# Kernel tuning notes

Measured on AMD Instinct MI355X. Metric: run time of the kernel, lower is better.

## Reference

```python
import jax, jax.numpy as jnp
import numpy as np

MARGIN = 0.3
EPS = 1e-12

def setup_inputs() -> dict:
    key = jax.random.key(0)
    k1, k2 = jax.random.split(key)
    B, D, NUM_IDS = 1024, 2048, 256
    features = jax.random.normal(k1, (B, D), dtype=jnp.float32)
    labels = jax.random.randint(k2, (B,), 0, NUM_IDS, dtype=jnp.int64)
    return {"features": features, "labels": labels}

def _pairwise_euclidean(features):
    # dist^2 = |x_i|^2 + |x_j|^2 - 2 x_i . x_j, clamped then sqrt (as in torch ref)
    sq = jnp.sum(features * features, axis=1)  # [B]
    d2 = sq[:, None] + sq[None, :] - 2.0 * (features @ features.T)
    return jnp.sqrt(jnp.maximum(d2, EPS))

def reference(features, labels):
    B = features.shape[0]
    dist = _pairwise_euclidean(features)  # [B, B]
    eq = labels[None, :] == labels[:, None]  # [B, B]; eq[i] == labels_equal row i
    eye = jnp.eye(B, dtype=bool)
    pos_mask = eq & ~eye
    neg_mask = ~eq
    neg_inf = jnp.float32(-jnp.inf)
    pos_inf = jnp.float32(jnp.inf)
    hardest_pos = jnp.max(jnp.where(pos_mask, dist, neg_inf), axis=1)  # [B]
    hardest_neg = jnp.min(jnp.where(neg_mask, dist, pos_inf), axis=1)  # [B]
    valid = jnp.any(pos_mask, axis=1) & jnp.any(neg_mask, axis=1)  # rows contributing a triplet
    per_row = jax.nn.relu(hardest_pos - hardest_neg + MARGIN)
    per_row = jnp.where(valid, per_row, 0.0)
    n_valid = jnp.sum(valid)
    loss = jnp.sum(per_row) / jnp.maximum(n_valid, 1).astype(per_row.dtype)
    num_active = jnp.sum(valid & (per_row > 0))
    return loss, num_active
```

## Files before the change

### kernel.cpp

```cpp
#include <hip/hip_runtime.h>
#include <math.h>

#define B_SZ 1024
#define D_SZ 2048
#define MARGIN 0.3f

typedef _Float16 f16x8 __attribute__((ext_vector_type(8)));
typedef float f32x16 __attribute__((ext_vector_type(16)));

union FragU { uint4 u; f16x8 v; };
union H4 { _Float16 h[4]; uint2 u; };



__global__ __launch_bounds__(256) void prep_kernel(const float* __restrict__ F,
                                                   _Float16* __restrict__ Fh,
                                                   float* __restrict__ sqpart,
                                                   int* __restrict__ hp,
                                                   int* __restrict__ hn,
                                                   int* __restrict__ flags) {
    __shared__ _Float16 slab[64][136];
    __shared__ float part[64];

    const int b = blockIdx.x;
    const int i = b >> 4;
    const int kseg = b & 15;
    const int t = threadIdx.x;
    const int lane = t & 63;
    const int w = t >> 6;

    const int idx = b * 256 + t;
    if (idx < 1024) {
        hp[idx] = 0;
        hn[idx] = 0x7F800000;
        flags[idx] = 0;
    }

#pragma unroll
    for (int q = 0; q < 8; ++q) {
        const int rl = q * 8 + (t >> 5);
        const int c4 = (t & 31) * 4;
        const float4 v = *(const float4*)(F + (size_t)(i * 64 + rl) * D_SZ +
                                          kseg * 128 + c4);
        float s = v.x * v.x + v.y * v.y + v.z * v.z + v.w * v.w;
#pragma unroll
        for (int mask = 1; mask < 32; mask <<= 1) s += __shfl_xor(s, mask);
        if ((t & 31) == 0) part[rl] = s;
        H4 p;
        p.h[0] = (_Float16)v.x; p.h[1] = (_Float16)v.y;
        p.h[2] = (_Float16)v.z; p.h[3] = (_Float16)v.w;
        *(uint2*)&slab[rl][c4] = p.u;
    }
    __syncthreads();

    if (t < 64) sqpart[kseg * 1024 + i * 64 + t] = part[t];

#pragma unroll
    for (int q2 = 0; q2 < 4; ++q2) {
        const int u = w * 4 + q2;
        const int kb = u >> 1;
        const int rg = u & 1;
        const uint4 d = *(const uint4*)&slab[rg * 32 + (lane & 31)]
                                          [kb * 16 + (lane >> 5) * 8];
        const size_t g = (size_t)((i * 128 + kseg * 8 + kb) * 2 + rg);
        *(uint4*)((char*)Fh + g * 1024 + (size_t)lane * 16) = d;
    }
}


__global__ __launch_bounds__(256, 2) void dist_f16_kernel(
    const _Float16* __restrict__ Fh, const int* __restrict__ labels,
    const float* __restrict__ sqpart, int* __restrict__ hp,
    int* __restrict__ hn, int* __restrict__ flags) {
    __shared__ __align__(16) char cb[32768];
    __shared__ int labR[64], labC[32];
    __shared__ float sqR[64], sqC[32];

    const int t = threadIdx.x;
    const int lane = t & 63;
    const int w = t >> 6;

    const int xcd = blockIdx.x & 7;
    const int cidx = blockIdx.x >> 3;
    const int bi = (xcd >> 1) * 4 + (cidx >> 4);
    const int bj = (xcd & 1) * 16 + (cidx & 15);
    const int rowBase = bi * 64, colBase = bj * 32;

    if (t < 64) {
        const int row = rowBase + t;
        float s = 0.f;
#pragma unroll
        for (int p = 0; p < 16; ++p) s += sqpart[p * 1024 + row];
        sqR[t] = s;
        labR[t] = labels[row];
    } else if (t < 96) {
        const int e = t - 64;
        const int row = colBase + e;
        float s = 0.f;
#pragma unroll
        for (int p = 0; p < 16; ++p) s += sqpart[p * 1024 + row];
        sqC[e] = s;
        labC[e] = labels[row];
    }
    __syncthreads();

    const char* __restrict__ FhB = (const char*)Fh;
    const char* pA0 = FhB + (size_t)((bi * 128 + w * 32) * 2) * 1024 + (size_t)lane * 16;
    const char* pB0 = FhB + (size_t)(((bj >> 1) * 128 + w * 32) * 2 + (bj & 1)) * 1024 +
                      (size_t)lane * 16;

    f32x16 acc[2];
#pragma unroll
    for (int a = 0; a < 2; ++a)
#pragma unroll
        for (int e = 0; e < 16; ++e) acc[a][e] = 0.f;

    auto LOADREG = [&](int s, uint4* r) {
        const size_t off = (size_t)s * 2048;
        r[0] = *(const uint4*)(pA0 + off);
        r[1] = *(const uint4*)(pA0 + off + 1024);
        r[2] = *(const uint4*)(pB0 + off);
    };
    auto MFMA2 = [&](const uint4* r) {
        FragU a0, a1, v0;
        a0.u = r[0];
        a1.u = r[1];
        v0.u = r[2];
        acc[0] = __builtin_amdgcn_mfma_f32_32x32x16_f16(a0.v, v0.v, acc[0], 0, 0, 0);
        acc[1] = __builtin_amdgcn_mfma_f32_32x32x16_f16(a1.v, v0.v, acc[1], 0, 0, 0);
    };

    uint4 ra[3], rb[3];
    LOADREG(0, ra);
#pragma unroll
    for (int s = 0; s < 32; s += 2) {
        LOADREG(s + 1, rb);
        MFMA2(ra);
        if (s + 2 < 32) LOADREG(s + 2, ra);
        MFMA2(rb);
    }

    __syncthreads();

#pragma unroll
    for (int fr = 0; fr < 2; ++fr)
#pragma unroll
        for (int g = 0; g < 4; ++g) {
            float4 v;
            v.x = acc[fr][g * 4 + 0];
            v.y = acc[fr][g * 4 + 1];
            v.z = acc[fr][g * 4 + 2];
            v.w = acc[fr][g * 4 + 3];
            *(float4*)(cb + (size_t)(w * 8192) +
                       (size_t)((fr * 4 + g) * 64 + lane) * 16) = v;
        }
    __syncthreads();

    if (w < 2) {
        const int fr = w;
        float cS[16];
#pragma unroll
        for (int e = 0; e < 16; ++e) cS[e] = 0.f;
#pragma unroll
        for (int wp = 0; wp < 4; ++wp)
#pragma unroll
            for (int g = 0; g < 4; ++g) {
                float4 v = *(const float4*)(cb + (size_t)(wp * 8192) +
                                            (size_t)((fr * 4 + g) * 64 + lane) * 16);
                cS[g * 4 + 0] += v.x;
                cS[g * 4 + 1] += v.y;
                cS[g * 4 + 2] += v.z;
                cS[g * 4 + 3] += v.w;
            }

        const float BIG = 1e38f;
        const int h = lane >> 5;
        const int colL = lane & 31;
        const int j = colBase + colL;
        const int lj = labC[colL];
        const float sqj = sqC[colL];
#pragma unroll
        for (int k = 0; k < 16; ++k) {
            const int rowL = fr * 32 + (k & 3) + 8 * (k >> 2) + 4 * h;
            const int i = rowBase + rowL;
            const float d2 = sqR[rowL] + sqj - 2.f * cS[k];
            const float d = sqrtf(fmaxf(d2, 1e-12f));
            const bool eq = (labR[rowL] == lj);
            const bool isPos = eq && (i != j);
            float pv = isPos ? d : -BIG;
            float nv = eq ? BIG : d;
            int pf = (isPos ? 1 : 0) | (eq ? 0 : 2);
#pragma unroll
            for (int mask = 1; mask < 32; mask <<= 1) {
                pv = fmaxf(pv, __shfl_xor(pv, mask));
                nv = fminf(nv, __shfl_xor(nv, mask));
                pf |= __shfl_xor(pf, mask);
            }
            if (colL == 0) {
                if (pf & 1) atomicMax(&hp[i], __float_as_int(pv));
                if (pf & 2) atomicMin(&hn[i], __float_as_int(nv));
                if (pf) atomicOr(&flags[i], pf);
            }
        }
    }
}


__global__ __launch_bounds__(1024) void final_kernel(const int* __restrict__ hp,
                                                     const int* __restrict__ hn,
                                                     const int* __restrict__ flags,
                                                     float* __restrict__ out) {
    __shared__ float ssum[16];
    __shared__ int svalid[16], sact[16];
    const int t = threadIdx.x;
    const float hpv = __int_as_float(hp[t]);
    const float hnv = __int_as_float(hn[t]);
    const int f = flags[t];
    const bool valid = (f == 3);
    float pr = fmaxf(hpv - hnv + MARGIN, 0.f);
    if (!valid) pr = 0.f;
    int act = (valid && pr > 0.f) ? 1 : 0;
    int vld = valid ? 1 : 0;
    float s = pr;
    for (int off = 32; off; off >>= 1) {
        s += __shfl_down(s, off);
        act += __shfl_down(act, off);
        vld += __shfl_down(vld, off);
    }
    if ((t & 63) == 0) {
        ssum[t >> 6] = s;
        svalid[t >> 6] = vld;
        sact[t >> 6] = act;
    }
    __syncthreads();
    if (t == 0) {
        float tot = 0.f;
        int nv = 0, na = 0;
#pragma unroll
        for (int i = 0; i < 16; ++i) {
            tot += ssum[i];
            nv += svalid[i];
            na += sact[i];
        }
        out[0] = tot / (float)(nv > 1 ? nv : 1);
        out[1] = (float)na;
    }
}


#define BM 64
#define BN 64
#define BK 32

__global__ __launch_bounds__(256) void sq_kernel(const float* __restrict__ F,
                                                 float* __restrict__ sq) {
    int row = blockIdx.x;
    const float4* r4 = (const float4*)(F + (size_t)row * D_SZ);
    int t = threadIdx.x;
    float s = 0.f;
#pragma unroll
    for (int q = 0; q < 2; ++q) {
        float4 v = r4[t + q * 256];
        s += v.x * v.x + v.y * v.y + v.z * v.z + v.w * v.w;
    }
    for (int off = 32; off; off >>= 1) s += __shfl_down(s, off);
    __shared__ float wsum[4];
    if ((t & 63) == 0) wsum[t >> 6] = s;
    __syncthreads();
    if (t == 0) sq[row] = wsum[0] + wsum[1] + wsum[2] + wsum[3];
}

__global__ __launch_bounds__(256) void init_kernel(int* __restrict__ hp,
                                                   int* __restrict__ hn,
                                                   int* __restrict__ flags) {
    int i = blockIdx.x * 256 + threadIdx.x;
    hp[i] = 0;
    hn[i] = 0x7F800000;
    flags[i] = 0;
}

__global__ __launch_bounds__(256) void dist_f32_kernel(
    const float* __restrict__ F, const int* __restrict__ labels,
    const float* __restrict__ sq, int* __restrict__ hp, int* __restrict__ hn,
    int* __restrict__ flags) {
    __shared__ float As[BK][BM];
    __shared__ float Bs[BK][BN];
    __shared__ int labR[BM], labC[BN];
    __shared__ float sqR[BM], sqC[BN];

    const int rowBase = blockIdx.y * BM;
    const int colBase = blockIdx.x * BN;
    const int t = threadIdx.x;
    const int tx = t & 15;
    const int ty = t >> 4;

    if (t < 64) {
        labR[t] = labels[rowBase + t];
        sqR[t] = sq[rowBase + t];
    } else if (t < 128) {
        int u = t - 64;
        labC[u] = labels[colBase + u];
        sqC[u] = sq[colBase + u];
    }

    float acc[4][4] = {{0.f}};
    const int m = t & 63;
    const int q = t >> 6;
    const float* aRow = F + (size_t)(rowBase + m) * D_SZ + q * 8;
    const float* bRow = F + (size_t)(colBase + m) * D_SZ + q * 8;

    for (int k0 = 0; k0 < D_SZ; k0 += BK) {
        float4 a0 = *(const float4*)(aRow + k0);
        float4 a1 = *(const float4*)(aRow + k0 + 4);
        float4 b0 = *(const float4*)(bRow + k0);
        float4 b1 = *(const float4*)(bRow + k0 + 4);
        __syncthreads();
        int kb = q * 8;
        As[kb + 0][m] = a0.x; As[kb + 1][m] = a0.y;
        As[kb + 2][m] = a0.z; As[kb + 3][m] = a0.w;
        As[kb + 4][m] = a1.x; As[kb + 5][m] = a1.y;
        As[kb + 6][m] = a1.z; As[kb + 7][m] = a1.w;
        Bs[kb + 0][m] = b0.x; Bs[kb + 1][m] = b0.y;
        Bs[kb + 2][m] = b0.z; Bs[kb + 3][m] = b0.w;
        Bs[kb + 4][m] = b1.x; Bs[kb + 5][m] = b1.y;
        Bs[kb + 6][m] = b1.z; Bs[kb + 7][m] = b1.w;
        __syncthreads();
#pragma unroll
        for (int kk = 0; kk < BK; ++kk) {
            float4 a = *(const float4*)&As[kk][ty * 4];
            float4 b = *(const float4*)&Bs[kk][tx * 4];
            acc[0][0] += a.x * b.x; acc[0][1] += a.x * b.y;
            acc[0][2] += a.x * b.z; acc[0][3] += a.x * b.w;
            acc[1][0] += a.y * b.x; acc[1][1] += a.y * b.y;
            acc[1][2] += a.y * b.z; acc[1][3] += a.y * b.w;
            acc[2][0] += a.z * b.x; acc[2][1] += a.z * b.y;
            acc[2][2] += a.z * b.z; acc[2][3] += a.z * b.w;
            acc[3][0] += a.w * b.x; acc[3][1] += a.w * b.y;
            acc[3][2] += a.w * b.z; acc[3][3] += a.w * b.w;
        }
    }

    float mp[4], mn[4];
    int pf[4];
#pragma unroll
    for (int rr = 0; rr < 4; ++rr) {
        const int i = rowBase + ty * 4 + rr;
        const int li = labR[ty * 4 + rr];
        const float si = sqR[ty * 4 + rr];
        mp[rr] = -3.4e38f;
        mn[rr] = 3.4e38f;
        pf[rr] = 0;
#pragma unroll
        for (int c = 0; c < 4; ++c) {
            const int j = colBase + tx * 4 + c;
            const float d2 = si + sqC[tx * 4 + c] - 2.f * acc[rr][c];
            const float dist = sqrtf(fmaxf(d2, 1e-12f));
            const bool eq = (li == labC[tx * 4 + c]);
            if (eq && (i != j)) {
                mp[rr] = fmaxf(mp[rr], dist);
                pf[rr] |= 1;
            }
            if (!eq) {
                mn[rr] = fminf(mn[rr], dist);
                pf[rr] |= 2;
            }
        }
    }
#pragma unroll
    for (int mask = 1; mask < 16; mask <<= 1)
#pragma unroll
        for (int rr = 0; rr < 4; ++rr) {
            mp[rr] = fmaxf(mp[rr], __shfl_xor(mp[rr], mask));
            mn[rr] = fminf(mn[rr], __shfl_xor(mn[rr], mask));
            pf[rr] |= __shfl_xor(pf[rr], mask);
        }
    if (tx == 0) {
#pragma unroll
        for (int rr = 0; rr < 4; ++rr) {
            const int i = rowBase + ty * 4 + rr;
            if (pf[rr] & 1) atomicMax(&hp[i], __float_as_int(mp[rr]));
            if (pf[rr] & 2) atomicMin(&hn[i], __float_as_int(mn[rr]));
            if (pf[rr]) atomicOr(&flags[i], pf[rr]);
        }
    }
}


extern "C" void kernel_launch(void* const* d_in, const int* in_sizes, int n_in,
                              void* d_out, int out_size, void* d_ws, size_t ws_size,
                              hipStream_t stream) {
    const float* F = (const float*)d_in[0];
    const int* labels = (const int*)d_in[1];
    float* out = (float*)d_out;
    char* ws = (char*)d_ws;

    const size_t FH = (size_t)B_SZ * D_SZ * 2;
    const size_t SQP = 16 * 1024 * sizeof(float);
    const size_t need = FH + SQP + 12 * 1024;

    if (ws_size >= need) {
        _Float16* Fh = (_Float16*)ws;
        float* sqpart = (float*)(ws + FH);
        char* tail = ws + FH + SQP;
        int* hp = (int*)tail;
        int* hn = (int*)(tail + 4096);
        int* flags = (int*)(tail + 8192);

        prep_kernel<<<256, 256, 0, stream>>>(F, Fh, sqpart, hp, hn, flags);
        dist_f16_kernel<<<512, 256, 0, stream>>>(Fh, labels, sqpart, hp, hn, flags);
        final_kernel<<<1, 1024, 0, stream>>>(hp, hn, flags, out);
    } else {
        float* sq = (float*)ws;
        int* hp = (int*)(ws + 4096);
        int* hn = (int*)(ws + 8192);
        int* flags = (int*)(ws + 12288);

        sq_kernel<<<B_SZ, 256, 0, stream>>>(F, sq);
        init_kernel<<<B_SZ / 256, 256, 0, stream>>>(hp, hn, flags);
        dim3 grid(B_SZ / BN, B_SZ / BM);
        dist_f32_kernel<<<grid, 256, 0, stream>>>(F, labels, sq, hp, hn, flags);
        final_kernel<<<1, 1024, 0, stream>>>(hp, hn, flags, out);
    }
}
```

Before: 32.28 us.

## Exploit distance symmetry by computing only upper-triangular 32x32 tiles

The distance kernel now computes only upper-triangular 32x32 tiles (528 blocks), each with a single MFMA accumulator per wave split over K. Each tile feeds both row reductions and column reductions into the per-row hardest positive and negative atomics, so the GEMM work is roughly halved. In exchange, tiles are smaller (64x32 before), each block loads two 32-row fragments instead of one 64-row and one 32-row, and column-side atomics are added. A serial loop maps the block id to a triangular (bi, bj) pair.

After: 33.04 us. +2.3%, slower.

```diff
diff --git a/kernel.cpp b/kernel.cpp
--- a/kernel.cpp
+++ b/kernel.cpp
@@ -68,33 +68,33 @@
 }
 
 
-__global__ __launch_bounds__(256, 2) void dist_f16_kernel(
+__global__ __launch_bounds__(256) void dist_f16_kernel(
     const _Float16* __restrict__ Fh, const int* __restrict__ labels,
     const float* __restrict__ sqpart, int* __restrict__ hp,
     int* __restrict__ hn, int* __restrict__ flags) {
-    __shared__ __align__(16) char cb[32768];
-    __shared__ int labR[64], labC[32];
-    __shared__ float sqR[64], sqC[32];
+    __shared__ __align__(16) float cbuf[3 * 1024];
+    __shared__ int labR[32], labC[32];
+    __shared__ float sqR[32], sqC[32];
 
     const int t = threadIdx.x;
     const int lane = t & 63;
     const int w = t >> 6;
 
-    const int xcd = blockIdx.x & 7;
-    const int cidx = blockIdx.x >> 3;
-    const int bi = (xcd >> 1) * 4 + (cidx >> 4);
-    const int bj = (xcd & 1) * 16 + (cidx & 15);
-    const int rowBase = bi * 64, colBase = bj * 32;
-
-    if (t < 64) {
+    const int tid = (blockIdx.x & 7) * 66 + (blockIdx.x >> 3);
+    int b = tid, bi = 0;
+    while (b >= 32 - bi) { b -= 32 - bi; ++bi; }
+    const int bj = bi + b;
+    const int rowBase = bi * 32, colBase = bj * 32;
+
+    if (t < 32) {
         const int row = rowBase + t;
         float s = 0.f;
 #pragma unroll
         for (int p = 0; p < 16; ++p) s += sqpart[p * 1024 + row];
         sqR[t] = s;
         labR[t] = labels[row];
-    } else if (t < 96) {
-        const int e = t - 64;
+    } else if (t < 64) {
+        const int e = t - 32;
         const int row = colBase + e;
         float s = 0.f;
 #pragma unroll
@@ -105,73 +105,65 @@
     __syncthreads();
 
     const char* __restrict__ FhB = (const char*)Fh;
-    const char* pA0 = FhB + (size_t)((bi * 128 + w * 32) * 2) * 1024 + (size_t)lane * 16;
-    const char* pB0 = FhB + (size_t)(((bj >> 1) * 128 + w * 32) * 2 + (bj & 1)) * 1024 +
+    const char* pA0 = FhB + (size_t)((bi >> 1) * 256 + w * 64 + (bi & 1)) * 1024 +
                       (size_t)lane * 16;
-
-    f32x16 acc[2];
-#pragma unroll
-    for (int a = 0; a < 2; ++a)
-#pragma unroll
-        for (int e = 0; e < 16; ++e) acc[a][e] = 0.f;
+    const char* pB0 = FhB + (size_t)((bj >> 1) * 256 + w * 64 + (bj & 1)) * 1024 +
+                      (size_t)lane * 16;
+
+    f32x16 acc;
+#pragma unroll
+    for (int e = 0; e < 16; ++e) acc[e] = 0.f;
 
     auto LOADREG = [&](int s, uint4* r) {
         const size_t off = (size_t)s * 2048;
         r[0] = *(const uint4*)(pA0 + off);
-        r[1] = *(const uint4*)(pA0 + off + 1024);
-        r[2] = *(const uint4*)(pB0 + off);
+        r[1] = *(const uint4*)(pB0 + off);
     };
-    auto MFMA2 = [&](const uint4* r) {
-        FragU a0, a1, v0;
-        a0.u = r[0];
-        a1.u = r[1];
-        v0.u = r[2];
-        acc[0] = __builtin_amdgcn_mfma_f32_32x32x16_f16(a0.v, v0.v, acc[0], 0, 0, 0);
-        acc[1] = __builtin_amdgcn_mfma_f32_32x32x16_f16(a1.v, v0.v, acc[1], 0, 0, 0);
+    auto MFMA1 = [&](const uint4* r) {
+        FragU a, v;
+        a.u = r[0];
+        v.u = r[1];
+        acc = __builtin_amdgcn_mfma_f32_32x32x16_f16(a.v, v.v, acc, 0, 0, 0);
     };
 
-    uint4 ra[3], rb[3];
+    uint4 ra[2], rb[2];
     LOADREG(0, ra);
 #pragma unroll
     for (int s = 0; s < 32; s += 2) {
         LOADREG(s + 1, rb);
-        MFMA2(ra);
+        MFMA1(ra);
         if (s + 2 < 32) LOADREG(s + 2, ra);
-        MFMA2(rb);
-    }
-
-    __syncthreads();
-
-#pragma unroll
-    for (int fr = 0; fr < 2; ++fr)
+        MFMA1(rb);
+    }
+
+    __syncthreads();
+    if (w > 0) {
+        float* r = cbuf + (w - 1) * 1024;
 #pragma unroll
         for (int g = 0; g < 4; ++g) {
             float4 v;
-            v.x = acc[fr][g * 4 + 0];
-            v.y = acc[fr][g * 4 + 1];
-            v.z = acc[fr][g * 4 + 2];
-            v.w = acc[fr][g * 4 + 3];
-            *(float4*)(cb + (size_t)(w * 8192) +
-                       (size_t)((fr * 4 + g) * 64 + lane) * 16) = v;
-        }
-    __syncthreads();
-
-    if (w < 2) {
-        const int fr = w;
-        float cS[16];
-#pragma unroll
-        for (int e = 0; e < 16; ++e) cS[e] = 0.f;
-#pragma unroll
-        for (int wp = 0; wp < 4; ++wp)
+            v.x = acc[g * 4 + 0];
+            v.y = acc[g * 4 + 1];
+            v.z = acc[g * 4 + 2];
+            v.w = acc[g * 4 + 3];
+            *(float4*)(r + (g * 64 + lane) * 4) = v;
+        }
+    }
+    __syncthreads();
+
+    if (w == 0) {
+#pragma unroll
+        for (int p = 0; p < 3; ++p) {
+            const float* r = cbuf + p * 1024;
 #pragma unroll
             for (int g = 0; g < 4; ++g) {
-                float4 v = *(const float4*)(cb + (size_t)(wp * 8192) +
-                                            (size_t)((fr * 4 + g) * 64 + lane) * 16);
-                cS[g * 4 + 0] += v.x;
-                cS[g * 4 + 1] += v.y;
-                cS[g * 4 + 2] += v.z;
-                cS[g * 4 + 3] += v.w;
+                float4 v = *(const float4*)(r + (g * 64 + lane) * 4);
+                acc[g * 4 + 0] += v.x;
+                acc[g * 4 + 1] += v.y;
+                acc[g * 4 + 2] += v.z;
+                acc[g * 4 + 3] += v.w;
             }
+        }
 
         const float BIG = 1e38f;
         const int h = lane >> 5;
@@ -179,17 +171,24 @@
         const int j = colBase + colL;
         const int lj = labC[colL];
         const float sqj = sqC[colL];
+        float cpv = -BIG, cnv = BIG;
+        int cpf = 0;
 #pragma unroll
         for (int k = 0; k < 16; ++k) {
-            const int rowL = fr * 32 + (k & 3) + 8 * (k >> 2) + 4 * h;
+            const int rowL = (k & 3) + 8 * (k >> 2) + 4 * h;
             const int i = rowBase + rowL;
-            const float d2 = sqR[rowL] + sqj - 2.f * cS[k];
+            const float d2 = sqR[rowL] + sqj - 2.f * acc[k];
             const float d = sqrtf(fmaxf(d2, 1e-12f));
             const bool eq = (labR[rowL] == lj);
             const bool isPos = eq && (i != j);
-            float pv = isPos ? d : -BIG;
-            float nv = eq ? BIG : d;
-            int pf = (isPos ? 1 : 0) | (eq ? 0 : 2);
+            const float pvi = isPos ? d : -BIG;
+            const float nvi = eq ? BIG : d;
+            const int pfi = (isPos ? 1 : 0) | (eq ? 0 : 2);
+            cpv = fmaxf(cpv, pvi);
+            cnv = fminf(cnv, nvi);
+            cpf |= pfi;
+            float pv = pvi, nv = nvi;
+            int pf = pfi;
 #pragma unroll
             for (int mask = 1; mask < 32; mask <<= 1) {
                 pv = fmaxf(pv, __shfl_xor(pv, mask));
@@ -201,6 +200,14 @@
                 if (pf & 2) atomicMin(&hn[i], __float_as_int(nv));
                 if (pf) atomicOr(&flags[i], pf);
             }
+        }
+        cpv = fmaxf(cpv, __shfl_xor(cpv, 32));
+        cnv = fminf(cnv, __shfl_xor(cnv, 32));
+        cpf |= __shfl_xor(cpf, 32);
+        if (h == 0) {
+            if (cpf & 1) atomicMax(&hp[j], __float_as_int(cpv));
+            if (cpf & 2) atomicMin(&hn[j], __float_as_int(cnv));
+            if (cpf) atomicOr(&flags[j], cpf);
         }
     }
 }
@@ -407,7 +414,7 @@
         int* flags = (int*)(tail + 8192);
 
         prep_kernel<<<256, 256, 0, stream>>>(F, Fh, sqpart, hp, hn, flags);
-        dist_f16_kernel<<<512, 256, 0, stream>>>(Fh, labels, sqpart, hp, hn, flags);
+        dist_f16_kernel<<<528, 256, 0, stream>>>(Fh, labels, sqpart, hp, hn, flags);
         final_kernel<<<1, 1024, 0, stream>>>(hp, hn, flags, out);
     } else {
         float* sq = (float*)ws;
```
